# Kernel optimization log

Measured on AMD Instinct MI355X. Metric: run time of the kernel, lower is better.

Reference implementation:

```python
import jax, jax.numpy as jnp
import numpy as np
from jax import lax

N = 8192

def _conv(x, w, b):
    # x: NCHW, w: OIHW, valid conv stride 1
    y = lax.conv_general_dilated(x, w, (1, 1), 'VALID',
                                 dimension_numbers=('NCHW', 'OIHW', 'NCHW'))
    return y + b[None, :, None, None]

def _maxpool2(x):
    return lax.reduce_window(x, -jnp.inf, lax.max, (1, 1, 2, 2), (1, 1, 2, 2), 'VALID')

def setup_inputs() -> dict:
    key = jax.random.key(0)
    ks = jax.random.split(key, 13)
    def rn(k, shape, scale):
        return jax.random.normal(k, shape, dtype=jnp.float32) * scale
    inp = {}
    inp['x'] = jax.random.normal(ks[0], (N, 3, 32, 32), dtype=jnp.float32)
    inp['W1'] = rn(ks[1], (6, 3, 5, 5), 0.1)
    inp['b1'] = rn(ks[2], (6,), 0.1)
    inp['W2'] = rn(ks[3], (16, 6, 5, 5), 0.08)
    inp['b2'] = rn(ks[4], (16,), 0.1)
    inp['Wf1'] = rn(ks[5], (120, 400), 0.05)
    inp['bf1'] = rn(ks[6], (120,), 0.05)
    inp['Wf2'] = rn(ks[7], (84, 120), 0.09)
    inp['bf2'] = rn(ks[8], (84,), 0.09)
    inp['Wg'] = rn(ks[9], (10, 84), 0.1)    # GATConv fc weight (no bias)
    inp['attn_l'] = rn(ks[10], (10,), 0.3)  # a_l (src)
    inp['attn_r'] = rn(ks[11], (10,), 0.3)  # a_r (dst)
    inp['bg'] = rn(ks[12], (10,), 0.1)      # GATConv output bias
    return inp

def reference(x, W1, b1, W2, b2, Wf1, bf1, Wf2, bf2, Wg, attn_l, attn_r, bg):
    # CNN feature extractor (LeNet style)
    h = _maxpool2(jax.nn.relu(_conv(x, W1, b1)))   # [N,6,14,14]
    h = _maxpool2(jax.nn.relu(_conv(h, W2, b2)))   # [N,16,5,5]
    h = h.reshape(-1, 16 * 5 * 5)                  # [N,400]
    h = jax.nn.relu(h @ Wf1.T + bf1)               # [N,120]
    h = jax.nn.relu(h @ Wf2.T + bf2)               # [N,84]
    # Single-head GAT over fully-connected graph (incl. self-loops):
    # equivalent dense formulation of DGL GATConv(84,10,1)
    z = h @ Wg.T                                    # [N,10]
    el = z @ attn_l                                 # src scores [N]
    er = z @ attn_r                                 # dst scores [N]
    # e[i,j]: edge src=j -> dst=i
    e = jax.nn.leaky_relu(er[:, None] + el[None, :], negative_slope=0.2)  # [N,N]
    alpha = jax.nn.softmax(e, axis=1)               # softmax over incoming edges
    out = alpha @ z + bg                            # [N,10]
    return out
```

## Files before the change

### kernel.cpp

```cpp
#include <hip/hip_runtime.h>
#include <hip/hip_bf16.h>

typedef _Float16 half8 __attribute__((ext_vector_type(8)));
typedef __attribute__((aligned(8))) half8 half8_a8;
typedef float floatx4 __attribute__((ext_vector_type(4)));

__device__ __forceinline__ float pool4_dpp(float v) {
  int s1 = __builtin_amdgcn_update_dpp(0, __float_as_int(v), 0xB1, 0xF, 0xF, true);
  float v1 = fmaxf(v, __int_as_float(s1));
  int s2 = __builtin_amdgcn_update_dpp(0, __float_as_int(v1), 0x4E, 0xF, 0xF, true);
  return fmaxf(v1, __int_as_float(s2));
}

__global__ __launch_bounds__(256) void k_prep(const float* __restrict__ Wf1,
    const float* __restrict__ Wf2, const float* __restrict__ Wg,
    const float* __restrict__ W1, const float* __restrict__ W2,
    _Float16* __restrict__ w1f, _Float16* __restrict__ w2f,
    _Float16* __restrict__ wgf, _Float16* __restrict__ B1,
    _Float16* __restrict__ B2M) {
  const int i = blockIdx.x * 256 + threadIdx.x;
  if (i < 53248) {
    const int n = i / 416, k = i - n * 416;
    w1f[i] = (_Float16)((n < 120 && k < 400) ? Wf1[n * 400 + k] : 0.f);
  } else if (i < 65536) {
    const int j = i - 53248;
    const int n = j >> 7, k = j & 127;
    w2f[j] = (_Float16)((n < 84 && k < 120) ? Wf2[n * 120 + k] : 0.f);
  } else if (i < 67072) {
    const int g = i - 65536;
    const int n = g / 96, k = g - n * 96;
    wgf[g] = (_Float16)((n < 10 && k < 84) ? Wg[n * 84 + k] : 0.f);
  } else if (i < 73216) {
    const int g = i - 67072;
    const int n = g / 192, k = g - n * 192;
    const int co = n >> 2, cy = (n >> 1) & 1, cx = n & 1;
    const int pidx = k >> 3, j = k & 7;
    const int r = pidx >> 2, ci = pidx & 3;
    float v = 0.f;
    if (co < 6 && ci < 3) {
      const int ky = r - cy, kx = j - cx;
      if (ky >= 0 && ky < 5 && kx >= 0 && kx < 5)
        v = W1[((co * 3 + ci) * 5 + ky) * 5 + kx];
    }
    B1[g] = (_Float16)v;
  } else if (i < 77312) {
    const int g = i - 73216;
    const int n = g >> 8, k = g & 255;
    float v = 0.f;
    if (k < 240) {
      const int ci = k / 40, rem = k - ci * 40, r = rem >> 3, j = rem & 7;
      if (j < 5) v = W2[((n * 6 + ci) * 5 + r) * 5 + j];
    }
    B2M[g] = (_Float16)v;
  }
}

__global__ __launch_bounds__(256) void k_conv1(const float* __restrict__ x,
    const _Float16* __restrict__ B1, const float* __restrict__ b1,
    _Float16* __restrict__ h1) {
  __shared__ __align__(16) char sm[31104];
  const int t = threadIdx.x;
  const int n0 = blockIdx.x * 2;
  const float4* x4 = (const float4*)(x + (size_t)n0 * 3072);
  for (int i = t; i < 1536; i += 256) {
    const float4 v = x4[i];
    const int img = i / 768, rem = i - img * 768;
    const int ci = rem >> 8, rem2 = rem & 255;
    const int y = rem2 >> 3, c = rem2 & 7;
    union { _Float16 h[2]; unsigned u; } p01, p23;
    p01.h[0] = (_Float16)v.x; p01.h[1] = (_Float16)v.y;
    p23.h[0] = (_Float16)v.z; p23.h[1] = (_Float16)v.w;
    char* row = sm + (img * 3 + ci) * 5184 + y * 80;
    *(uint2*)(row + 8 * c) = make_uint2(p01.u, p23.u);
    *(unsigned*)(row + 2596 + 8 * c) = p01.u;
    *(unsigned*)(row + 2600 + 8 * c) = p23.u;
  }
  if (t < 192) {
    const int img = t / 96, r2 = t - img * 96, ci = r2 >> 5, y = r2 & 31;
    *(unsigned*)(sm + (img * 3 + ci) * 5184 + 2596 + y * 80 + 64) = 0u;
  }
  __syncthreads();
  const int w4 = t >> 6, lane = t & 63;
  const int l16 = lane & 15, q = lane >> 4;
  const int px = l16;
  const int colOff = (px & 1) ? (2596 + 4 * px) : (4 * px);
  const char* base = sm + ((q == 3) ? 0 : q * 5184) + colOff;
  half8 bfr[2][6];
#pragma unroll
  for (int nt = 0; nt < 2; nt++)
#pragma unroll
    for (int kc = 0; kc < 6; kc++)
      bfr[nt][kc] =
          *(const half8*)(B1 + (size_t)(nt * 16 + l16) * 192 + kc * 32 + q * 8);
  const int co_n = l16 >> 2;
  const int co1 = 4 + co_n;
  const float bias0 = b1[co_n];
  const float bias1 = (co1 < 6) ? b1[co1] : 0.f;
  const int img_w = w4 >> 1, pyh = w4 & 1;
  const int py0 = pyh * 7;
  const char* ibase = base + img_w * 15552;
  half8 a[6];
#pragma unroll
  for (int r = 0; r < 6; r++)
    a[r] = *(const half8_a8*)(ibase + (2 * py0 + r) * 80);
  const size_t ob = (size_t)(n0 + img_w) * 1176;
  const bool store_lane = (l16 & 3) == 0;
  for (int it = 0; it < 7; ++it) {
    const int py = py0 + it;
    floatx4 acc0, acc1;
#pragma unroll
    for (int r = 0; r < 4; r++) { acc0[r] = 0.f; acc1[r] = 0.f; }
#pragma unroll
    for (int kc = 0; kc < 6; kc++) {
      acc0 = __builtin_amdgcn_mfma_f32_16x16x32_f16(a[kc], bfr[0][kc], acc0, 0, 0, 0);
      acc1 = __builtin_amdgcn_mfma_f32_16x16x32_f16(a[kc], bfr[1][kc], acc1, 0, 0, 0);
    }
    if (it < 6) {
      a[0] = a[2]; a[1] = a[3]; a[2] = a[4]; a[3] = a[5];
      a[4] = *(const half8_a8*)(ibase + (2 * py + 6) * 80);
      a[5] = *(const half8_a8*)(ibase + (2 * py + 7) * 80);
    }
    float p0[4], p1[4];
#pragma unroll
    for (int r = 0; r < 4; r++) {
      p0[r] = fmaxf(pool4_dpp(acc0[r]) + bias0, 0.f);
      p1[r] = fmaxf(pool4_dpp(acc1[r]) + bias1, 0.f);
    }
    if (store_lane) {
      union { _Float16 h[2]; unsigned u; } s01, s23;
      s01.h[0] = (_Float16)p0[0]; s01.h[1] = (_Float16)p0[1];
      s23.h[0] = (_Float16)p0[2]; s23.h[1] = (_Float16)p0[3];
      _Float16* dst = h1 + ob + co_n * 196 + py * 14 + q * 4;
      *(unsigned*)dst = s01.u;
      if (q < 3) *(unsigned*)(dst + 2) = s23.u;
      if (co1 < 6) {
        union { _Float16 h[2]; unsigned u; } t01, t23;
        t01.h[0] = (_Float16)p1[0]; t01.h[1] = (_Float16)p1[1];
        t23.h[0] = (_Float16)p1[2]; t23.h[1] = (_Float16)p1[3];
        _Float16* dst1 = h1 + ob + co1 * 196 + py * 14 + q * 4;
        *(unsigned*)dst1 = t01.u;
        if (q < 3) *(unsigned*)(dst1 + 2) = t23.u;
      }
    }
  }
}

__global__ __launch_bounds__(256) void k_conv2(const _Float16* __restrict__ h1,
    const _Float16* __restrict__ B2M, const float* __restrict__ b2,
    _Float16* __restrict__ h2) {
  __shared__ __align__(16) char sm[22272];
  const int t = threadIdx.x;
  const int n0 = blockIdx.x * 2;
  if (t < 168) {
    const int img = t / 84, rem = t - img * 84;
    const int ci = rem / 14, y = rem - ci * 14;
    const unsigned* src =
        (const unsigned*)(h1 + (size_t)(n0 + img) * 1176 + ci * 196 + y * 14);
    unsigned u[10];
#pragma unroll
    for (int k = 0; k < 7; k++) u[k] = src[k];
    u[7] = 0u; u[8] = 0u; u[9] = 0u;
    char* base = sm + img * 11136 + ci * 1856 + y * 32;
#pragma unroll
    for (int ww = 0; ww < 8; ww++) {
      *(unsigned*)(base + 4 * ww) = u[ww];
      *(unsigned*)(base + 464 + 4 * ww) = (u[ww] >> 16) | (u[ww + 1] << 16);
      *(unsigned*)(base + 928 + 4 * ww) = u[ww + 1];
      *(unsigned*)(base + 1392 + 4 * ww) = (u[ww + 1] >> 16) | (u[ww + 2] << 16);
    }
  }
  if (t < 32) {
    const int im = t >> 4;
    h2[(size_t)(n0 + im) * 416 + 400 + (t & 15)] = (_Float16)0.f;
  }
  __syncthreads();
  const int w = t >> 6, lane = t & 63;
  const int l16 = lane & 15, q = lane >> 4;
  int C2[8];
#pragma unroll
  for (int kc = 0; kc < 8; kc++) {
    const int pidx = kc * 4 + q;
    C2[kc] = (pidx < 30) ? (pidx / 5) * 1856 + (pidx % 5) * 32 : 0;
  }
  half8 bfr[8];
#pragma unroll
  for (int kc = 0; kc < 8; kc++)
    bfr[kc] = *(const half8*)(B2M + (size_t)l16 * 256 + kc * 32 + q * 8);
  const float bias = b2[l16];
  for (int mt = w; mt < 13; mt += 4) {
    const int m = min(mt * 16 + l16, 199);
    const int pos = m >> 2, cy = (m >> 1) & 1, cx = m & 1;
    const int img = pos / 25, p = pos - img * 25;
    const int py = p / 5, px = p - py * 5;
    const int h = 2 * px + cx, s = h & 3;
    const char* base =
        sm + img * 11136 + s * 464 + (2 * py + cy) * 32 + (h - s) * 2;
    half8 a[8];
#pragma unroll
    for (int kc = 0; kc < 8; kc++) a[kc] = *(const half8_a8*)(base + C2[kc]);
    floatx4 acc;
#pragma unroll
    for (int r = 0; r < 4; r++) acc[r] = 0.f;
#pragma unroll
    for (int kc = 0; kc < 8; kc++)
      acc = __builtin_amdgcn_mfma_f32_16x16x32_f16(a[kc], bfr[kc], acc, 0, 0, 0);
    const float v = fmaxf(fmaxf(acc[0], acc[1]), fmaxf(acc[2], acc[3]));
    const int posL = mt * 4 + q;
    if (posL < 50) {
      const int im = posL / 25, pp = posL - im * 25;
      h2[(size_t)(n0 + im) * 416 + l16 * 25 + pp] =
          (_Float16)fmaxf(v + bias, 0.f);
    }
  }
}

__global__ __launch_bounds__(256) void k_mlp(
    const _Float16* __restrict__ h2, const _Float16* __restrict__ w1,
    const float* __restrict__ bf1, const _Float16* __restrict__ w2,
    const float* __restrict__ bf2, const _Float16* __restrict__ wg,
    const float* __restrict__ al, const float* __restrict__ ar,
    float* __restrict__ z, float* __restrict__ el, float* __restrict__ er) {
  __shared__ __align__(16) _Float16 h3s[32 * 136];
  __shared__ __align__(16) _Float16 h4s[32 * 104];
  __shared__ float zs[32 * 17];
  const int t = threadIdx.x;
  const int w = t >> 6, lane = t & 63;
  const int l16 = lane & 15, q = lane >> 4;
  const int row0 = blockIdx.x * 32;
  for (int i = t; i < 2176; i += 256) ((float*)h3s)[i] = 0.f;
  for (int i = t; i < 1664; i += 256) ((float*)h4s)[i] = 0.f;
  const int rt = w & 1, cg = w >> 1;
  const int am = row0 + rt * 16 + l16;
  floatx4 acc[4];
#pragma unroll
  for (int ct = 0; ct < 4; ct++)
#pragma unroll
    for (int r = 0; r < 4; r++) acc[ct][r] = 0.f;
  const half8* Ag = (const half8*)(h2 + (size_t)am * 416 + q * 8);
  for (int kc = 0; kc < 13; kc++) {
    half8 a = Ag[kc * 4];
#pragma unroll
    for (int ct = 0; ct < 4; ct++) {
      const int n = cg * 64 + ct * 16 + l16;
      half8 b = *(const half8*)(w1 + (size_t)n * 416 + kc * 32 + q * 8);
      acc[ct] = __builtin_amdgcn_mfma_f32_16x16x32_f16(a, b, acc[ct], 0, 0, 0);
    }
  }
  __syncthreads();
#pragma unroll
  for (int ct = 0; ct < 4; ct++) {
    const int n = cg * 64 + ct * 16 + l16;
    if (n < 120) {
      const float bias = bf1[n];
#pragma unroll
      for (int r = 0; r < 4; r++) {
        const int rr = rt * 16 + q * 4 + r;
        h3s[rr * 136 + n] = (_Float16)fmaxf(acc[ct][r] + bias, 0.f);
      }
    }
  }
  __syncthreads();
  const int cbase2 = (w >> 1) * 3;
  floatx4 acc2[3];
#pragma unroll
  for (int ct = 0; ct < 3; ct++)
#pragma unroll
    for (int r = 0; r < 4; r++) acc2[ct][r] = 0.f;
  const _Float16* A2 = h3s + (rt * 16 + l16) * 136 + q * 8;
  for (int kc = 0; kc < 4; kc++) {
    half8 a = *(const half8*)(A2 + kc * 32);
#pragma unroll
    for (int ct = 0; ct < 3; ct++) {
      const int n = (cbase2 + ct) * 16 + l16;
      half8 b = *(const half8*)(w2 + (size_t)n * 128 + kc * 32 + q * 8);
      acc2[ct] = __builtin_amdgcn_mfma_f32_16x16x32_f16(a, b, acc2[ct], 0, 0, 0);
    }
  }
  __syncthreads();
#pragma unroll
  for (int ct = 0; ct < 3; ct++) {
    const int n = (cbase2 + ct) * 16 + l16;
    if (n < 84) {
      const float bias = bf2[n];
#pragma unroll
      for (int r = 0; r < 4; r++) {
        const int rr = rt * 16 + q * 4 + r;
        h4s[rr * 104 + n] = (_Float16)fmaxf(acc2[ct][r] + bias, 0.f);
      }
    }
  }
  __syncthreads();
  if (w < 2) {
    floatx4 acc3;
#pragma unroll
    for (int r = 0; r < 4; r++) acc3[r] = 0.f;
    const _Float16* A3 = h4s + (w * 16 + l16) * 104 + q * 8;
    for (int kc = 0; kc < 3; kc++) {
      half8 a = *(const half8*)(A3 + kc * 32);
      half8 b = *(const half8*)(wg + (size_t)l16 * 96 + kc * 32 + q * 8);
      acc3 = __builtin_amdgcn_mfma_f32_16x16x32_f16(a, b, acc3, 0, 0, 0);
    }
#pragma unroll
    for (int r = 0; r < 4; r++) {
      const int rr = w * 16 + q * 4 + r;
      zs[rr * 17 + l16] = acc3[r];
      if (l16 < 10) z[(size_t)(row0 + rr) * 10 + l16] = acc3[r];
    }
  }
  __syncthreads();
  if (t < 32) {
    float e1 = 0.f, e2 = 0.f;
#pragma unroll
    for (int d = 0; d < 10; d++) {
      const float zv = zs[t * 17 + d];
      e1 += zv * al[d];
      e2 += zv * ar[d];
    }
    el[row0 + t] = e1;
    er[row0 + t] = e2;
  }
}

__global__ __launch_bounds__(256) void k_elmax(const float* __restrict__ el,
                                               float* __restrict__ out) {
  __shared__ float red[4];
  const int t = threadIdx.x;
  float m = -1e30f;
  for (int i = t; i < 8192; i += 256) m = fmaxf(m, el[i]);
#pragma unroll
  for (int off = 32; off > 0; off >>= 1) m = fmaxf(m, __shfl_down(m, off, 64));
  if ((t & 63) == 0) red[t >> 6] = m;
  __syncthreads();
  if (t == 0) out[0] = fmaxf(fmaxf(red[0], red[1]), fmaxf(red[2], red[3]));
}

__global__ __launch_bounds__(256) void k_attn(const float* __restrict__ z,
    const float* __restrict__ el, const float* __restrict__ er,
    const float* __restrict__ elmax, float* __restrict__ part) {
  __shared__ __align__(16) float zsm[256 * 12];
  const int t = threadIdx.x;
  const int split = blockIdx.y;
  const int jbase = split * 256;
  for (int idx = t; idx < 2560; idx += 256) {
    int jj = idx / 10, d = idx - jj * 10;
    zsm[jj * 12 + d] = z[(size_t)jbase * 10 + idx];
  }
  zsm[t * 12 + 10] = el[jbase + t];
  const int i0 = blockIdx.x * 1024 + t;
  const float mx = elmax[0];
  float eri[4], mi[4];
#pragma unroll
  for (int g = 0; g < 4; g++) {
    eri[g] = er[i0 + g * 256];
    const float s0 = eri[g] + mx;
    mi[g] = fmaxf(s0, 0.2f * s0);
  }
  float num[4][10];
#pragma unroll
  for (int g = 0; g < 4; g++)
#pragma unroll
    for (int d = 0; d < 10; d++) num[g][d] = 0.f;
  float den[4] = {0.f, 0.f, 0.f, 0.f};
  __syncthreads();
#pragma unroll 2
  for (int jj = 0; jj < 256; jj++) {
    const float4 za = *(const float4*)(zsm + jj * 12);
    const float4 zb = *(const float4*)(zsm + jj * 12 + 4);
    const float4 zc = *(const float4*)(zsm + jj * 12 + 8);
    const float elj = zc.z;
#pragma unroll
    for (int g = 0; g < 4; g++) {
      const float s2 = eri[g] + elj;
      const float lr = fmaxf(s2, 0.2f * s2);
      const float wgt = __expf(lr - mi[g]);
      den[g] += wgt;
      num[g][0] += wgt * za.x; num[g][1] += wgt * za.y;
      num[g][2] += wgt * za.z; num[g][3] += wgt * za.w;
      num[g][4] += wgt * zb.x; num[g][5] += wgt * zb.y;
      num[g][6] += wgt * zb.z; num[g][7] += wgt * zb.w;
      num[g][8] += wgt * zc.x; num[g][9] += wgt * zc.y;
    }
  }
#pragma unroll
  for (int g = 0; g < 4; g++) {
    float* pp = part + (size_t)split * 98304 + i0 + g * 256;
#pragma unroll
    for (int d = 0; d < 10; d++) pp[d * 8192] = num[g][d];
    pp[10 * 8192] = den[g];
  }
}

__global__ __launch_bounds__(256) void k_final(const float* __restrict__ part,
    const float* __restrict__ bg, float* __restrict__ out) {
  __shared__ float red[8][32][12];
  const int t = threadIdx.x;
  const int i0 = blockIdx.x * 32;
  const int il = t & 31, sg = t >> 5;
  float v[11];
#pragma unroll
  for (int d = 0; d < 11; d++) v[d] = 0.f;
  for (int u = 0; u < 4; u++) {
    const float* pp = part + (size_t)(sg * 4 + u) * 98304 + i0 + il;
#pragma unroll
    for (int d = 0; d < 11; d++) v[d] += pp[d * 8192];
  }
#pragma unroll
  for (int d = 0; d < 11; d++) red[sg][il][d] = v[d];
  __syncthreads();
  for (int t2 = t; t2 < 352; t2 += 256) {
    const int ii = t2 / 11, d = t2 - ii * 11;
    if (d < 10) {
      float num = 0.f, den = 0.f;
#pragma unroll
      for (int s = 0; s < 8; s++) {
        num += red[s][ii][d];
        den += red[s][ii][10];
      }
      out[(size_t)(i0 + ii) * 10 + d] = num / den + bg[d];
    }
  }
}

extern "C" void kernel_launch(void* const* d_in, const int* in_sizes, int n_in,
                              void* d_out, int out_size, void* d_ws, size_t ws_size,
                              hipStream_t stream) {
  const float* x   = (const float*)d_in[0];
  const float* W1  = (const float*)d_in[1];
  const float* b1  = (const float*)d_in[2];
  const float* W2  = (const float*)d_in[3];
  const float* b2  = (const float*)d_in[4];
  const float* Wf1 = (const float*)d_in[5];
  const float* bf1 = (const float*)d_in[6];
  const float* Wf2 = (const float*)d_in[7];
  const float* bf2 = (const float*)d_in[8];
  const float* Wg  = (const float*)d_in[9];
  const float* al  = (const float*)d_in[10];
  const float* ar  = (const float*)d_in[11];
  const float* bg  = (const float*)d_in[12];
  float* out = (float*)d_out;

  float* ws = (float*)d_ws;
  _Float16* h1f = (_Float16*)ws;
  float* p = ws + (size_t)8192 * 588;
  _Float16* h2f = (_Float16*)p;
  p += (size_t)8192 * 208;
  float* z   = p; p += (size_t)8192 * 10;
  float* el  = p; p += 8192;
  float* er  = p; p += 8192;
  float* emx = p; p += 16;
  _Float16* w1f = (_Float16*)p; p += 26624;
  _Float16* w2f = (_Float16*)p; p += 6144;
  _Float16* wgf = (_Float16*)p; p += 768;
  _Float16* B1g = (_Float16*)p; p += 3072;
  _Float16* B2g = (_Float16*)p; p += 2048;
  float* part = ws;

  k_prep<<<302, 256, 0, stream>>>(Wf1, Wf2, Wg, W1, W2, w1f, w2f, wgf, B1g, B2g);
  k_conv1<<<4096, 256, 0, stream>>>(x, B1g, b1, h1f);
  k_conv2<<<4096, 256, 0, stream>>>(h1f, B2g, b2, h2f);
  k_mlp<<<256, 256, 0, stream>>>(h2f, w1f, bf1, w2f, bf2, wgf, al, ar, z, el, er);
  k_elmax<<<1, 256, 0, stream>>>(el, emx);
  dim3 ag(8, 32);
  k_attn<<<ag, 256, 0, stream>>>(z, el, er, emx, part);
  k_final<<<256, 256, 0, stream>>>(part, bg, out);
}
```

Before: 286.6 us.

## Compute GAT attention aggregation with fp16 MFMA and exp2, one image per conv1 block

```diff
diff --git a/kernel.cpp b/kernel.cpp
--- a/kernel.cpp
+++ b/kernel.cpp
@@ -4,6 +4,8 @@
 typedef _Float16 half8 __attribute__((ext_vector_type(8)));
 typedef __attribute__((aligned(8))) half8 half8_a8;
 typedef float floatx4 __attribute__((ext_vector_type(4)));
+
+#define LOG2E 1.44269504088896340736f
 
 __device__ __forceinline__ float pool4_dpp(float v) {
   int s1 = __builtin_amdgcn_update_dpp(0, __float_as_int(v), 0xB1, 0xF, 0xF, true);
@@ -58,26 +60,24 @@
 __global__ __launch_bounds__(256) void k_conv1(const float* __restrict__ x,
     const _Float16* __restrict__ B1, const float* __restrict__ b1,
     _Float16* __restrict__ h1) {
-  __shared__ __align__(16) char sm[31104];
-  const int t = threadIdx.x;
-  const int n0 = blockIdx.x * 2;
-  const float4* x4 = (const float4*)(x + (size_t)n0 * 3072);
-  for (int i = t; i < 1536; i += 256) {
+  __shared__ __align__(16) char sm[15552];
+  const int t = threadIdx.x;
+  const float4* x4 = (const float4*)(x + (size_t)blockIdx.x * 3072);
+  for (int i = t; i < 768; i += 256) {
     const float4 v = x4[i];
-    const int img = i / 768, rem = i - img * 768;
-    const int ci = rem >> 8, rem2 = rem & 255;
+    const int ci = i >> 8, rem2 = i & 255;
     const int y = rem2 >> 3, c = rem2 & 7;
     union { _Float16 h[2]; unsigned u; } p01, p23;
     p01.h[0] = (_Float16)v.x; p01.h[1] = (_Float16)v.y;
     p23.h[0] = (_Float16)v.z; p23.h[1] = (_Float16)v.w;
-    char* row = sm + (img * 3 + ci) * 5184 + y * 80;
+    char* row = sm + ci * 5184 + y * 80;
     *(uint2*)(row + 8 * c) = make_uint2(p01.u, p23.u);
     *(unsigned*)(row + 2596 + 8 * c) = p01.u;
     *(unsigned*)(row + 2600 + 8 * c) = p23.u;
   }
-  if (t < 192) {
-    const int img = t / 96, r2 = t - img * 96, ci = r2 >> 5, y = r2 & 31;
-    *(unsigned*)(sm + (img * 3 + ci) * 5184 + 2596 + y * 80 + 64) = 0u;
+  if (t < 96) {
+    const int ci = t >> 5, y = t & 31;
+    *(unsigned*)(sm + ci * 5184 + 2596 + y * 80 + 64) = 0u;
   }
   __syncthreads();
   const int w4 = t >> 6, lane = t & 63;
@@ -96,17 +96,15 @@
   const int co1 = 4 + co_n;
   const float bias0 = b1[co_n];
   const float bias1 = (co1 < 6) ? b1[co1] : 0.f;
-  const int img_w = w4 >> 1, pyh = w4 & 1;
-  const int py0 = pyh * 7;
-  const char* ibase = base + img_w * 15552;
+  const int py0 = (7 * w4) >> 1;
+  const int py1 = (7 * (w4 + 1)) >> 1;
   half8 a[6];
 #pragma unroll
   for (int r = 0; r < 6; r++)
-    a[r] = *(const half8_a8*)(ibase + (2 * py0 + r) * 80);
-  const size_t ob = (size_t)(n0 + img_w) * 1176;
+    a[r] = *(const half8_a8*)(base + (2 * py0 + r) * 80);
+  const size_t ob = (size_t)blockIdx.x * 1176;
   const bool store_lane = (l16 & 3) == 0;
-  for (int it = 0; it < 7; ++it) {
-    const int py = py0 + it;
+  for (int py = py0; py < py1; ++py) {
     floatx4 acc0, acc1;
 #pragma unroll
     for (int r = 0; r < 4; r++) { acc0[r] = 0.f; acc1[r] = 0.f; }
@@ -115,10 +113,10 @@
       acc0 = __builtin_amdgcn_mfma_f32_16x16x32_f16(a[kc], bfr[0][kc], acc0, 0, 0, 0);
       acc1 = __builtin_amdgcn_mfma_f32_16x16x32_f16(a[kc], bfr[1][kc], acc1, 0, 0, 0);
     }
-    if (it < 6) {
+    if (py < py1 - 1) {
       a[0] = a[2]; a[1] = a[3]; a[2] = a[4]; a[3] = a[5];
-      a[4] = *(const half8_a8*)(ibase + (2 * py + 6) * 80);
-      a[5] = *(const half8_a8*)(ibase + (2 * py + 7) * 80);
+      a[4] = *(const half8_a8*)(base + (2 * py + 6) * 80);
+      a[5] = *(const half8_a8*)(base + (2 * py + 7) * 80);
     }
     float p0[4], p1[4];
 #pragma unroll
@@ -219,7 +217,7 @@
     const float* __restrict__ bf1, const _Float16* __restrict__ w2,
     const float* __restrict__ bf2, const _Float16* __restrict__ wg,
     const float* __restrict__ al, const float* __restrict__ ar,
-    float* __restrict__ z, float* __restrict__ el, float* __restrict__ er) {
+    _Float16* __restrict__ zT, float* __restrict__ el, float* __restrict__ er) {
   __shared__ __align__(16) _Float16 h3s[32 * 136];
   __shared__ __align__(16) _Float16 h4s[32 * 104];
   __shared__ float zs[32 * 17];
@@ -304,7 +302,6 @@
     for (int r = 0; r < 4; r++) {
       const int rr = w * 16 + q * 4 + r;
       zs[rr * 17 + l16] = acc3[r];
-      if (l16 < 10) z[(size_t)(row0 + rr) * 10 + l16] = acc3[r];
     }
   }
   __syncthreads();
@@ -316,8 +313,13 @@
       e1 += zv * al[d];
       e2 += zv * ar[d];
     }
-    el[row0 + t] = e1;
-    er[row0 + t] = e2;
+    el[row0 + t] = e1 * LOG2E;
+    er[row0 + t] = e2 * LOG2E;
+  }
+  for (int idx = t; idx < 352; idx += 256) {
+    const int d = idx >> 5, c = idx & 31;
+    zT[(size_t)d * 8192 + row0 + c] =
+        (d < 10) ? (_Float16)zs[c * 17 + d] : (_Float16)1.0f;
   }
 }
 
@@ -334,59 +336,44 @@
   if (t == 0) out[0] = fmaxf(fmaxf(red[0], red[1]), fmaxf(red[2], red[3]));
 }
 
-__global__ __launch_bounds__(256) void k_attn(const float* __restrict__ z,
+__global__ __launch_bounds__(256) void k_attn(const _Float16* __restrict__ zT,
     const float* __restrict__ el, const float* __restrict__ er,
     const float* __restrict__ elmax, float* __restrict__ part) {
-  __shared__ __align__(16) float zsm[256 * 12];
-  const int t = threadIdx.x;
-  const int split = blockIdx.y;
-  const int jbase = split * 256;
-  for (int idx = t; idx < 2560; idx += 256) {
-    int jj = idx / 10, d = idx - jj * 10;
-    zsm[jj * 12 + d] = z[(size_t)jbase * 10 + idx];
-  }
-  zsm[t * 12 + 10] = el[jbase + t];
-  const int i0 = blockIdx.x * 1024 + t;
+  const int t = threadIdx.x;
+  const int w = t >> 6, lane = t & 63;
+  const int l16 = lane & 15, q = lane >> 4;
+  const int itile = blockIdx.x * 64 + w * 16;
+  const int jb = blockIdx.y * 1024;
   const float mx = elmax[0];
-  float eri[4], mi[4];
-#pragma unroll
-  for (int g = 0; g < 4; g++) {
-    eri[g] = er[i0 + g * 256];
-    const float s0 = eri[g] + mx;
-    mi[g] = fmaxf(s0, 0.2f * s0);
-  }
-  float num[4][10];
-#pragma unroll
-  for (int g = 0; g < 4; g++)
-#pragma unroll
-    for (int d = 0; d < 10; d++) num[g][d] = 0.f;
-  float den[4] = {0.f, 0.f, 0.f, 0.f};
-  __syncthreads();
-#pragma unroll 2
-  for (int jj = 0; jj < 256; jj++) {
-    const float4 za = *(const float4*)(zsm + jj * 12);
-    const float4 zb = *(const float4*)(zsm + jj * 12 + 4);
-    const float4 zc = *(const float4*)(zsm + jj * 12 + 8);
-    const float elj = zc.z;
-#pragma unroll
-    for (int g = 0; g < 4; g++) {
-      const float s2 = eri[g] + elj;
-      const float lr = fmaxf(s2, 0.2f * s2);
-      const float wgt = __expf(lr - mi[g]);
-      den[g] += wgt;
-      num[g][0] += wgt * za.x; num[g][1] += wgt * za.y;
-      num[g][2] += wgt * za.z; num[g][3] += wgt * za.w;
-      num[g][4] += wgt * zb.x; num[g][5] += wgt * zb.y;
-      num[g][6] += wgt * zb.z; num[g][7] += wgt * zb.w;
-      num[g][8] += wgt * zc.x; num[g][9] += wgt * zc.y;
-    }
-  }
-#pragma unroll
-  for (int g = 0; g < 4; g++) {
-    float* pp = part + (size_t)split * 98304 + i0 + g * 256;
-#pragma unroll
-    for (int d = 0; d < 10; d++) pp[d * 8192] = num[g][d];
-    pp[10 * 8192] = den[g];
+  const float eri = er[itile + l16];
+  const float s0 = eri + mx;
+  const float mi = fmaxf(s0, 0.2f * s0);
+  floatx4 acc;
+#pragma unroll
+  for (int r = 0; r < 4; r++) acc[r] = 0.f;
+  const float* elp = el + jb + q * 8;
+  const _Float16* ztp = zT + (size_t)l16 * 8192 + jb + q * 8;
+  for (int jc = 0; jc < 32; jc++) {
+    const float4 e0 = *(const float4*)(elp + jc * 32);
+    const float4 e1 = *(const float4*)(elp + jc * 32 + 4);
+    float wf[8];
+    const float ej[8] = {e0.x, e0.y, e0.z, e0.w, e1.x, e1.y, e1.z, e1.w};
+#pragma unroll
+    for (int u = 0; u < 8; u++) {
+      const float s = eri + ej[u];
+      const float lr = fmaxf(s, 0.2f * s);
+      wf[u] = exp2f(lr - mi);
+    }
+    half8 a;
+#pragma unroll
+    for (int u = 0; u < 8; u++) a[u] = (_Float16)wf[u];
+    const half8 b = *(const half8*)(ztp + jc * 32);
+    acc = __builtin_amdgcn_mfma_f32_16x16x32_f16(a, b, acc, 0, 0, 0);
+  }
+  if (l16 < 11) {
+    float* pp = part + (size_t)blockIdx.y * 98304 + (size_t)l16 * 8192 + itile + q * 4;
+#pragma unroll
+    for (int r = 0; r < 4; r++) pp[r] = acc[r];
   }
 }
 
@@ -396,16 +383,9 @@
   const int t = threadIdx.x;
   const int i0 = blockIdx.x * 32;
   const int il = t & 31, sg = t >> 5;
-  float v[11];
-#pragma unroll
-  for (int d = 0; d < 11; d++) v[d] = 0.f;
-  for (int u = 0; u < 4; u++) {
-    const float* pp = part + (size_t)(sg * 4 + u) * 98304 + i0 + il;
-#pragma unroll
-    for (int d = 0; d < 11; d++) v[d] += pp[d * 8192];
-  }
-#pragma unroll
-  for (int d = 0; d < 11; d++) red[sg][il][d] = v[d];
+  const float* pp = part + (size_t)sg * 98304 + i0 + il;
+#pragma unroll
+  for (int d = 0; d < 11; d++) red[sg][il][d] = pp[d * 8192];
   __syncthreads();
   for (int t2 = t; t2 < 352; t2 += 256) {
     const int ii = t2 / 11, d = t2 - ii * 11;
@@ -444,7 +424,7 @@
   float* p = ws + (size_t)8192 * 588;
   _Float16* h2f = (_Float16*)p;
   p += (size_t)8192 * 208;
-  float* z   = p; p += (size_t)8192 * 10;
+  _Float16* zTf = (_Float16*)p; p += 65536;
   float* el  = p; p += 8192;
   float* er  = p; p += 8192;
   float* emx = p; p += 16;
@@ -456,11 +436,11 @@
   float* part = ws;
 
   k_prep<<<302, 256, 0, stream>>>(Wf1, Wf2, Wg, W1, W2, w1f, w2f, wgf, B1g, B2g);
-  k_conv1<<<4096, 256, 0, stream>>>(x, B1g, b1, h1f);
+  k_conv1<<<8192, 256, 0, stream>>>(x, B1g, b1, h1f);
   k_conv2<<<4096, 256, 0, stream>>>(h1f, B2g, b2, h2f);
-  k_mlp<<<256, 256, 0, stream>>>(h2f, w1f, bf1, w2f, bf2, wgf, al, ar, z, el, er);
+  k_mlp<<<256, 256, 0, stream>>>(h2f, w1f, bf1, w2f, bf2, wgf, al, ar, zTf, el, er);
   k_elmax<<<1, 256, 0, stream>>>(el, emx);
-  dim3 ag(8, 32);
-  k_attn<<<ag, 256, 0, stream>>>(z, el, er, emx, part);
+  dim3 ag(128, 8);
+  k_attn<<<ag, 256, 0, stream>>>(zTf, el, er, emx, part);
   k_final<<<256, 256, 0, stream>>>(part, bg, out);
 }
```

After: 284.4 us. Within noise of the previous version (-0.8%).
